# Kernel tuning notes

Hardware: AMD Instinct MI355X
Metric: run time of the kernel (lower is better)

Reference implementation:

```python
import jax, jax.numpy as jnp
import numpy as np

N_EMBD = 1024
N_HEAD = 16
HEAD_DIM = N_EMBD // N_HEAD

def setup_inputs() -> dict:
    key = jax.random.key(0)
    ks = jax.random.split(key, 5)
    B, T, C = 2, 2048, N_EMBD
    s = 1.0 / np.sqrt(C)
    x = jax.random.normal(ks[0], (B, T, C), dtype=jnp.float32)
    W_qkv = jax.random.normal(ks[1], (C, 3 * C), dtype=jnp.float32) * s
    b_qkv = jax.random.normal(ks[2], (3 * C,), dtype=jnp.float32) * 0.02
    W_o = jax.random.normal(ks[3], (C, C), dtype=jnp.float32) * s
    b_o = jax.random.normal(ks[4], (C,), dtype=jnp.float32) * 0.02
    return {"x": x, "W_qkv": W_qkv, "b_qkv": b_qkv, "W_o": W_o, "b_o": b_o}

def reference(x, W_qkv, b_qkv, W_o, b_o):
    B, T, C = x.shape
    H, D = N_HEAD, HEAD_DIM
    scale = 1.0 / np.sqrt(D)
    qkv = jnp.einsum('btc,cf->btf', x, W_qkv) + b_qkv  # [B,T,3C]
    q, k, v = jnp.split(qkv, 3, axis=-1)
    # [B,H,T,D]
    q = q.reshape(B, T, H, D).transpose(0, 2, 1, 3)
    k = k.reshape(B, T, H, D).transpose(0, 2, 1, 3)
    v = v.reshape(B, T, H, D).transpose(0, 2, 1, 3)
    att = jnp.einsum('bhqd,bhkd->bhqk', q, k) * scale  # [B,H,T,T]
    causal = jnp.tril(jnp.ones((T, T), dtype=bool))
    att = jnp.where(causal[None, None], att, -jnp.inf)
    att = jax.nn.softmax(att, axis=-1)
    y = jnp.einsum('bhqk,bhkd->bhqd', att, v)  # [B,H,T,D]
    y = y.transpose(0, 2, 1, 3).reshape(B, T, C)
    return jnp.einsum('btc,cf->btf', y, W_o) + b_o
```

## Files before the change

### kernel.cpp

```cpp
#include <hip/hip_runtime.h>
#include <hip/hip_bf16.h>

#define TT 2048
#define BB 2
#define CC 1024
#define NH 16
#define HD 64

typedef __attribute__((ext_vector_type(8))) short short8;
typedef __attribute__((ext_vector_type(4))) short short4b;
typedef __attribute__((ext_vector_type(4))) float f32x4;

typedef unsigned int __attribute__((address_space(1))) ui_gas;
typedef unsigned int __attribute__((address_space(3))) ui_las;

__device__ __forceinline__ float us2f(unsigned short u) {
    union { unsigned int i; float f; } v; v.i = ((unsigned int)u) << 16; return v.f;
}
__device__ __forceinline__ unsigned short f2us(float f) {
    union { float f; unsigned int i; } v; v.f = f;
    unsigned int i = v.i;
    unsigned int lsb = (i >> 16) & 1u;
    i += 0x7fffu + lsb;
    return (unsigned short)(i >> 16);
}
__device__ __forceinline__ unsigned int pack2_trunc(float a, float b) {
    union { float f; unsigned int u; } x, y; x.f = a; y.f = b;
    return (y.u & 0xffff0000u) | (x.u >> 16);
}

__device__ __forceinline__ void gl_lds16(const unsigned short* g, unsigned short* l) {
    __builtin_amdgcn_global_load_lds((const ui_gas*)g, (ui_las*)l, 16, 0, 0);
}

__global__ __launch_bounds__(64) void detect_kernel(
    const void* p0, const void* p1, const void* p2, const void* p3, const void* p4,
    int* flags)
{
    const void* ps[5] = {p0, p1, p2, p3, p4};
    const int lane = threadIdx.x;
    for (int k = 0; k < 5; ++k) {
        const unsigned short* u = (const unsigned short*)ps[k];
        int bad = 0;
        #pragma unroll
        for (int j = 0; j < 4; ++j) {
            float v = us2f(u[lane * 4 + j]);
            if (!(fabsf(v) < 1e4f)) bad = 1;
        }
        unsigned long long m = __ballot(bad != 0);
        if (lane == 0) flags[k] = (__popcll(m) < 4) ? 1 : 0;
    }
}

__device__ __forceinline__ float4 load4(const void* p, size_t i, int isbf) {
    if (isbf) {
        ushort4 u = *reinterpret_cast<const ushort4*>((const unsigned short*)p + i);
        return make_float4(us2f(u.x), us2f(u.y), us2f(u.z), us2f(u.w));
    } else {
        return *reinterpret_cast<const float4*>((const float*)p + i);
    }
}
__device__ __forceinline__ float load1(const void* p, size_t i, int isbf) {
    return isbf ? us2f(((const unsigned short*)p)[i]) : ((const float*)p)[i];
}

__global__ __launch_bounds__(256) void convert_bf16(
    const void* __restrict__ X, unsigned short* __restrict__ Y,
    const int* __restrict__ flags, int fi)
{
    const int isbf = flags[fi];
    const size_t i = ((size_t)blockIdx.x * 256 + threadIdx.x) * 8;
    float4 a = load4(X, i, isbf);
    float4 b = load4(X, i + 4, isbf);
    alignas(16) unsigned short pk[8];
    pk[0] = f2us(a.x); pk[1] = f2us(a.y); pk[2] = f2us(a.z); pk[3] = f2us(a.w);
    pk[4] = f2us(b.x); pk[5] = f2us(b.y); pk[6] = f2us(b.z); pk[7] = f2us(b.w);
    *reinterpret_cast<uint4*>(Y + i) = *reinterpret_cast<const uint4*>(pk);
}

__global__ __launch_bounds__(256) void transpose_w(
    const void* __restrict__ W, unsigned short* __restrict__ Wt,
    int Krows, int N, const int* __restrict__ flags, int fi)
{
    const int isbf = flags[fi];
    __shared__ float Ls[64 * 65];
    const int t = threadIdx.x;
    const int n0 = blockIdx.x * 64, k0 = blockIdx.y * 64;
    {
        const int r = t >> 2, cq = (t & 3) << 4;
        #pragma unroll
        for (int i = 0; i < 4; ++i) {
            float4 v = load4(W, (size_t)(k0 + r) * N + n0 + cq + i * 4, isbf);
            Ls[r * 65 + cq + i * 4 + 0] = v.x;
            Ls[r * 65 + cq + i * 4 + 1] = v.y;
            Ls[r * 65 + cq + i * 4 + 2] = v.z;
            Ls[r * 65 + cq + i * 4 + 3] = v.w;
        }
    }
    __syncthreads();
    {
        const int c = t & 63, kg = (t >> 6) * 16;
        alignas(16) unsigned short pk[16];
        #pragma unroll
        for (int i = 0; i < 16; ++i) pk[i] = f2us(Ls[(kg + i) * 65 + c]);
        unsigned short* dst = Wt + (size_t)(n0 + c) * Krows + k0 + kg;
        *reinterpret_cast<uint4*>(dst + 0) = *reinterpret_cast<const uint4*>(&pk[0]);
        *reinterpret_cast<uint4*>(dst + 8) = *reinterpret_cast<const uint4*>(&pk[8]);
    }
}

__global__ __launch_bounds__(256) void gemm_mfma(
    const unsigned short* __restrict__ A,
    const unsigned short* __restrict__ Bt,
    const void* __restrict__ bias, void* __restrict__ C,
    int M, int N, int K,
    const int* __restrict__ flags, int biasfi, int cfi)
{
    const int bias_bf = (biasfi >= 0) ? flags[biasfi] : 0;
    const int c_bf    = (cfi >= 0) ? flags[cfi] : ((cfi == -2) ? 1 : 0);

    __shared__ __align__(16) unsigned short Asl[8 * 512];
    __shared__ __align__(16) unsigned short Bsl[8 * 512];

    const int tid = threadIdx.x;
    const int l  = tid & 63;
    const int w  = tid >> 6;
    const int wm = w >> 1, wn = w & 1;
    const int bm = blockIdx.y * 128, bn = blockIdx.x * 128;
    const int lm = l & 15;
    const int lk = (l >> 4) * 8;

    f32x4 acc[4][4];
    #pragma unroll
    for (int i = 0; i < 4; ++i)
        #pragma unroll
        for (int j = 0; j < 4; ++j) acc[i][j] = (f32x4){0.f, 0.f, 0.f, 0.f};

    for (int k0 = 0; k0 < K; k0 += 32) {
        #pragma unroll
        for (int s = 0; s < 2; ++s) {
            const int r = 2 * w + s;
            gl_lds16(A  + (size_t)(bm + r * 16 + lm) * K + k0 + lk, &Asl[r * 512]);
            gl_lds16(Bt + (size_t)(bn + r * 16 + lm) * K + k0 + lk, &Bsl[r * 512]);
        }
        __syncthreads();
        short8 af[4], bf[4];
        #pragma unroll
        for (int i = 0; i < 4; ++i)
            af[i] = *reinterpret_cast<const short8*>(&Asl[(4 * wm + i) * 512 + l * 8]);
        #pragma unroll
        for (int j = 0; j < 4; ++j)
            bf[j] = *reinterpret_cast<const short8*>(&Bsl[(4 * wn + j) * 512 + l * 8]);
        #pragma unroll
        for (int i = 0; i < 4; ++i)
            #pragma unroll
            for (int j = 0; j < 4; ++j)
                acc[i][j] = __builtin_amdgcn_mfma_f32_16x16x32_bf16(af[i], bf[j], acc[i][j], 0, 0, 0);
        __syncthreads();
    }

    const int quad = l >> 4;
    float bv[4];
    #pragma unroll
    for (int j = 0; j < 4; ++j) bv[j] = load1(bias, bn + wn * 64 + j * 16 + lm, bias_bf);

    #pragma unroll
    for (int i = 0; i < 4; ++i) {
        #pragma unroll
        for (int r = 0; r < 4; ++r) {
            const int row = bm + wm * 64 + i * 16 + quad * 4 + r;
            #pragma unroll
            for (int j = 0; j < 4; ++j) {
                const int col = bn + wn * 64 + j * 16 + lm;
                const float val = acc[i][j][r] + bv[j];
                if (c_bf) ((unsigned short*)C)[(size_t)row * N + col] = f2us(val);
                else      ((float*)C)[(size_t)row * N + col] = val;
            }
        }
    }
}

__global__ __launch_bounds__(256) void transpose_v(
    const unsigned short* __restrict__ qkv, unsigned short* __restrict__ Vt)
{
    __shared__ __align__(16) unsigned short Ls[64 * 72];
    const int tid = threadIdx.x;
    const int tt = blockIdx.x;
    const int bh = blockIdx.y;
    const int b = bh >> 4, h = bh & 15;
    {
        const int tok = tid & 63, w = tid >> 6;
        const unsigned short* src = qkv + (size_t)(b * TT + tt * 64 + tok) * 3 * CC + 2 * CC + h * HD;
        #pragma unroll
        for (int c2 = 0; c2 < 2; ++c2) {
            int c = 2 * w + c2;
            uint4 d = *(const uint4*)(src + c * 8);
            *(uint4*)(&Ls[tok * 72 + c * 8]) = d;
        }
    }
    __syncthreads();
    {
        const int d = tid >> 2, kq = tid & 3;
        unsigned short out[16];
        #pragma unroll
        for (int i = 0; i < 16; ++i) out[i] = Ls[(kq * 16 + i) * 72 + d];
        unsigned short* dst = Vt + (size_t)bh * HD * TT + (size_t)d * TT + tt * 64 + kq * 16;
        *(uint4*)(dst + 0) = *(uint4*)(&out[0]);
        *(uint4*)(dst + 8) = *(uint4*)(&out[8]);
    }
}

__global__ __launch_bounds__(256) void attn_mfma(
    const unsigned short* __restrict__ qkv,
    const unsigned short* __restrict__ Vt,
    unsigned short* __restrict__ y)
{
    __shared__ __align__(16) unsigned short Ksh[8 * 512];
    __shared__ __align__(16) unsigned short Vsh[1039 * 8];

    const int tid = threadIdx.x;
    const int l   = tid & 63;
    const int w   = tid >> 6;
    const int quad = l >> 4;
    const int col  = l & 15;

    const int n  = blockIdx.x;
    const int g  = n >> 3;
    const int bh = (n & 7) * 4 + (g & 3);
    const int i  = g >> 2;
    const int tA = i, tB = 31 - i;
    const int b  = bh >> 4, h = bh & 15;

    for (int s = tid; s < 1039; s += 256)
        *(uint2*)(&Vsh[s * 8 + 4]) = make_uint2(0u, 0u);

    const float QSCALE = 0.18033688f;
    short8 qfA[2], qfB[2];
    #pragma unroll
    for (int t2 = 0; t2 < 2; ++t2) {
        const int qt = t2 ? tB : tA;
        short8* qf = t2 ? qfB : qfA;
        const int token = qt * 64 + w * 16 + col;
        const unsigned short* qrow = qkv + (size_t)(b * TT + token) * 3 * CC + h * HD;
        #pragma unroll
        for (int ks = 0; ks < 2; ++ks) {
            ushort4 u0 = *(const ushort4*)(qrow + ks * 32 + quad * 8);
            ushort4 u1 = *(const ushort4*)(qrow + ks * 32 + quad * 8 + 4);
            alignas(16) unsigned short pk[8];
            pk[0] = f2us(us2f(u0.x) * QSCALE);
            pk[1] = f2us(us2f(u0.y) * QSCALE);
            pk[2] = f2us(us2f(u0.z) * QSCALE);
            pk[3] = f2us(us2f(u0.w) * QSCALE);
            pk[4] = f2us(us2f(u1.x) * QSCALE);
            pk[5] = f2us(us2f(u1.y) * QSCALE);
            pk[6] = f2us(us2f(u1.z) * QSCALE);
            pk[7] = f2us(us2f(u1.w) * QSCALE);
            qf[ks] = *(const short8*)pk;
        }
    }

    f32x4 oA[4], oB[4];
    #pragma unroll
    for (int nb = 0; nb < 4; ++nb) {
        oA[nb] = (f32x4){0.f, 0.f, 0.f, 0.f};
        oB[nb] = (f32x4){0.f, 0.f, 0.f, 0.f};
    }
    float mA = -3e38f, lAc = 0.f, mB = -3e38f, lBc = 0.f;

    const unsigned short* kbase = qkv + (size_t)b * TT * 3 * CC + CC + h * HD;
    const unsigned short* vbase = Vt + (size_t)bh * HD * TT;

    const int vd = tid >> 2, vg0 = (tid & 3) * 4;

    uint4 rk[2], rv[2];
    auto issue_loads = [&](int kt) {
        const unsigned short* ksrc = kbase + (size_t)(kt * 64 + l) * 3 * CC;
        #pragma unroll
        for (int c2 = 0; c2 < 2; ++c2) {
            const int c = 2 * w + c2;
            rk[c2] = *(const uint4*)(ksrc + c * 8);
        }
        const unsigned short* vsrc = vbase + (size_t)vd * TT + kt * 64 + vg0 * 4;
        rv[0] = *(const uint4*)(vsrc + 0);
        rv[1] = *(const uint4*)(vsrc + 8);
    };
    auto write_lds = [&]() {
        #pragma unroll
        for (int c2 = 0; c2 < 2; ++c2) {
            const int c = 2 * w + c2;
            const int ks = c >> 2, q = c & 3;
            const int slot = ((quad * 2 + ks) * 64 + q * 16 + col) * 8;
            *(uint4*)(&Ksh[slot]) = rk[c2];
        }
        *(uint2*)(&Vsh[((vg0 + 0) * 65 + vd) * 8]) = make_uint2(rv[0].x, rv[0].y);
        *(uint2*)(&Vsh[((vg0 + 1) * 65 + vd) * 8]) = make_uint2(rv[0].z, rv[0].w);
        *(uint2*)(&Vsh[((vg0 + 2) * 65 + vd) * 8]) = make_uint2(rv[1].x, rv[1].y);
        *(uint2*)(&Vsh[((vg0 + 3) * 65 + vd) * 8]) = make_uint2(rv[1].z, rv[1].w);
    };

    auto step = [&](const short8* qf, f32x4* o, float& m_i, float& l_i, bool diag) {
        f32x4 st[4];
        #pragma unroll
        for (int nb = 0; nb < 4; ++nb) {
            f32x4 acc = {0.f, 0.f, 0.f, 0.f};
            #pragma unroll
            for (int ks = 0; ks < 2; ++ks) {
                short8 kf = *(const short8*)(&Ksh[((nb * 2 + ks) * 64 + l) * 8]);
                acc = __builtin_amdgcn_mfma_f32_16x16x32_bf16(kf, qf[ks], acc, 0, 0, 0);
            }
            st[nb] = acc;
        }
        float sv[4][4];
        #pragma unroll
        for (int nb = 0; nb < 4; ++nb)
            #pragma unroll
            for (int r = 0; r < 4; ++r) {
                float v = st[nb][r];
                if (diag && (nb * 16 + quad * 4 + r > w * 16 + col)) v = -3e38f;
                sv[nb][r] = v;
            }
        float rm = sv[0][0];
        #pragma unroll
        for (int nb = 0; nb < 4; ++nb)
            #pragma unroll
            for (int r = 0; r < 4; ++r) rm = fmaxf(rm, sv[nb][r]);
        rm = fmaxf(rm, __shfl_xor(rm, 16));
        rm = fmaxf(rm, __shfl_xor(rm, 32));
        const float mn = fmaxf(m_i, rm);
        const float al = __builtin_exp2f(m_i - mn);
        float pv[4][4];
        float rs = 0.f;
        #pragma unroll
        for (int nb = 0; nb < 4; ++nb)
            #pragma unroll
            for (int r = 0; r < 4; ++r) {
                float p = __builtin_exp2f(sv[nb][r] - mn);
                pv[nb][r] = p;
                rs += p;
            }
        rs += __shfl_xor(rs, 16);
        rs += __shfl_xor(rs, 32);
        l_i = l_i * al + rs;
        m_i = mn;
        float alr[4];
        #pragma unroll
        for (int r = 0; r < 4; ++r) alr[r] = __shfl(al, quad * 4 + r);
        #pragma unroll
        for (int nb = 0; nb < 4; ++nb)
            #pragma unroll
            for (int r = 0; r < 4; ++r) o[nb][r] *= alr[r];
#if __has_builtin(__builtin_amdgcn_mfma_f32_16x16x16bf16_1k)
        short4b pf[4];
        #pragma unroll
        for (int nbk = 0; nbk < 4; ++nbk) {
            union { short4b s; unsigned int u[2]; } pk;
            pk.u[0] = pack2_trunc(pv[nbk][0], pv[nbk][1]);
            pk.u[1] = pack2_trunc(pv[nbk][2], pv[nbk][3]);
            pf[nbk] = pk.s;
        }
        #pragma unroll
        for (int nbd = 0; nbd < 4; ++nbd)
            #pragma unroll
            for (int nbk = 0; nbk < 4; ++nbk) {
                short4b vf = *(const short4b*)(&Vsh[((nbk * 4 + quad) * 65 + nbd * 16 + col) * 8]);
                o[nbd] = __builtin_amdgcn_mfma_f32_16x16x16bf16_1k(pf[nbk], vf, o[nbd], 0, 0, 0);
            }
#else
        short8 pf[4];
        #pragma unroll
        for (int nbk = 0; nbk < 4; ++nbk) {
            union { short8 s; unsigned int u[4]; } pk;
            pk.u[0] = pack2_trunc(pv[nbk][0], pv[nbk][1]);
            pk.u[1] = pack2_trunc(pv[nbk][2], pv[nbk][3]);
            pk.u[2] = 0u; pk.u[3] = 0u;
            pf[nbk] = pk.s;
        }
        #pragma unroll
        for (int nbd = 0; nbd < 4; ++nbd)
            #pragma unroll
            for (int nbk = 0; nbk < 4; ++nbk) {
                short8 vf = *(const short8*)(&Vsh[((nbk * 4 + quad) * 65 + nbd * 16 + col) * 8]);
                o[nbd] = __builtin_amdgcn_mfma_f32_16x16x32_bf16(pf[nbk], vf, o[nbd], 0, 0, 0);
            }
#endif
    };

    issue_loads(0);
    for (int kt = 0; kt <= tB; ++kt) {
        write_lds();
        __syncthreads();
        if (kt < tB) issue_loads(kt + 1);
        step(qfB, oB, mB, lBc, kt == tB);
        if (kt <= tA) step(qfA, oA, mA, lAc, kt == tA);
        __syncthreads();
    }

    #pragma unroll
    for (int t2 = 0; t2 < 2; ++t2) {
        const int qt = t2 ? tB : tA;
        f32x4* o = t2 ? oB : oA;
        const float inv = 1.f / (t2 ? lBc : lAc);
        float invr[4];
        #pragma unroll
        for (int r = 0; r < 4; ++r) invr[r] = __shfl(inv, quad * 4 + r);
        #pragma unroll
        for (int nb = 0; nb < 4; ++nb)
            #pragma unroll
            for (int r = 0; r < 4; ++r) {
                int token = qt * 64 + w * 16 + quad * 4 + r;
                y[(size_t)(b * TT + token) * CC + h * HD + nb * 16 + col] = f2us(o[nb][r] * invr[r]);
            }
    }
}

extern "C" void kernel_launch(void* const* d_in, const int* in_sizes, int n_in,
                              void* d_out, int out_size, void* d_ws, size_t ws_size,
                              hipStream_t stream) {
    const int M = BB * TT;

    char* ws = (char*)d_ws;
    int*            flags = (int*)ws;                         ws += 256;
    unsigned short* xb    = (unsigned short*)ws;              ws += (size_t)M * CC * 2;
    unsigned short* Wqkvt = (unsigned short*)ws;              ws += (size_t)3 * CC * CC * 2;
    unsigned short* Wot   = (unsigned short*)ws;              ws += (size_t)CC * CC * 2;
    unsigned short* qkv   = (unsigned short*)ws;              ws += (size_t)M * 3 * CC * 2;
    unsigned short* Vt    = (unsigned short*)ws;              ws += (size_t)BB * NH * HD * TT * 2;
    unsigned short* y     = (unsigned short*)ws;

    detect_kernel<<<1, 64, 0, stream>>>(d_in[0], d_in[1], d_in[2], d_in[3], d_in[4], flags);

    convert_bf16<<<(M * CC) / (256 * 8), 256, 0, stream>>>(d_in[0], xb, flags, 0);
    transpose_w<<<dim3(3 * CC / 64, CC / 64), 256, 0, stream>>>(d_in[1], Wqkvt, CC, 3 * CC, flags, 1);
    transpose_w<<<dim3(CC / 64, CC / 64), 256, 0, stream>>>(d_in[3], Wot, CC, CC, flags, 3);

    gemm_mfma<<<dim3(3 * CC / 128, M / 128), 256, 0, stream>>>(
        xb, Wqkvt, d_in[2], qkv, M, 3 * CC, CC, flags, 2, -2);

    transpose_v<<<dim3(TT / 64, BB * NH), 256, 0, stream>>>(qkv, Vt);

    attn_mfma<<<512, 256, 0, stream>>>(qkv, Vt, y);

    gemm_mfma<<<dim3(CC / 128, M / 128), 256, 0, stream>>>(
        y, Wot, d_in[4], d_out, M, CC, CC, flags, 4, 0);
}
```

Measured before the change: 248.5 us.

## Split attention into one q-tile per block and retile output-projection GEMM

Attention blocks previously paired a short and a long query tile (i and 31-i) for load balance. Now each block handles a single query tile, doubling the grid to 1024 blocks, ordered longest-first. The V LDS buffer is halved when the 16x16x16 MFMA path is available, and the output-projection GEMM is templated to use 128x64 tiles so it launches more blocks. The goal is more parallelism and occupancy. The trade-off is that K/V tiles are reloaded per query tile instead of shared across two tiles.

```diff
diff --git a/kernel.cpp b/kernel.cpp
--- a/kernel.cpp
+++ b/kernel.cpp
@@ -13,6 +13,12 @@
 
 typedef unsigned int __attribute__((address_space(1))) ui_gas;
 typedef unsigned int __attribute__((address_space(3))) ui_las;
+
+#if __has_builtin(__builtin_amdgcn_mfma_f32_16x16x16bf16_1k)
+#define PV16 1
+#else
+#define PV16 0
+#endif
 
 __device__ __forceinline__ float us2f(unsigned short u) {
     union { unsigned int i; float f; } v; v.i = ((unsigned int)u) << 16; return v.f;
@@ -109,6 +115,7 @@
     }
 }
 
+template<int WM, int WN, int NWM, int NWN>
 __global__ __launch_bounds__(256) void gemm_mfma(
     const unsigned short* __restrict__ A,
     const unsigned short* __restrict__ Bt,
@@ -116,62 +123,69 @@
     int M, int N, int K,
     const int* __restrict__ flags, int biasfi, int cfi)
 {
+    constexpr int BM = WM * 16 * NWM, BN = WN * 16 * NWN;
+    constexpr int ASL = BM / 16, BSL = BN / 16;
+
     const int bias_bf = (biasfi >= 0) ? flags[biasfi] : 0;
     const int c_bf    = (cfi >= 0) ? flags[cfi] : ((cfi == -2) ? 1 : 0);
 
-    __shared__ __align__(16) unsigned short Asl[8 * 512];
-    __shared__ __align__(16) unsigned short Bsl[8 * 512];
+    __shared__ __align__(16) unsigned short Asl[ASL * 512];
+    __shared__ __align__(16) unsigned short Bsl[BSL * 512];
 
     const int tid = threadIdx.x;
     const int l  = tid & 63;
     const int w  = tid >> 6;
-    const int wm = w >> 1, wn = w & 1;
-    const int bm = blockIdx.y * 128, bn = blockIdx.x * 128;
+    const int wm = w / NWN, wn = w % NWN;
+    const int bm = blockIdx.y * BM, bn = blockIdx.x * BN;
     const int lm = l & 15;
     const int lk = (l >> 4) * 8;
 
-    f32x4 acc[4][4];
+    f32x4 acc[WM][WN];
     #pragma unroll
-    for (int i = 0; i < 4; ++i)
-        #pragma unroll
-        for (int j = 0; j < 4; ++j) acc[i][j] = (f32x4){0.f, 0.f, 0.f, 0.f};
+    for (int i = 0; i < WM; ++i)
+        #pragma unroll
+        for (int j = 0; j < WN; ++j) acc[i][j] = (f32x4){0.f, 0.f, 0.f, 0.f};
 
     for (int k0 = 0; k0 < K; k0 += 32) {
         #pragma unroll
-        for (int s = 0; s < 2; ++s) {
-            const int r = 2 * w + s;
-            gl_lds16(A  + (size_t)(bm + r * 16 + lm) * K + k0 + lk, &Asl[r * 512]);
+        for (int s = 0; s < ASL / 4; ++s) {
+            const int r = w * (ASL / 4) + s;
+            gl_lds16(A + (size_t)(bm + r * 16 + lm) * K + k0 + lk, &Asl[r * 512]);
+        }
+        #pragma unroll
+        for (int s = 0; s < BSL / 4; ++s) {
+            const int r = w * (BSL / 4) + s;
             gl_lds16(Bt + (size_t)(bn + r * 16 + lm) * K + k0 + lk, &Bsl[r * 512]);
         }
         __syncthreads();
-        short8 af[4], bf[4];
-        #pragma unroll
-        for (int i = 0; i < 4; ++i)
-            af[i] = *reinterpret_cast<const short8*>(&Asl[(4 * wm + i) * 512 + l * 8]);
-        #pragma unroll
-        for (int j = 0; j < 4; ++j)
-            bf[j] = *reinterpret_cast<const short8*>(&Bsl[(4 * wn + j) * 512 + l * 8]);
-        #pragma unroll
-        for (int i = 0; i < 4; ++i)
-            #pragma unroll
-            for (int j = 0; j < 4; ++j)
+        short8 af[WM], bf[WN];
+        #pragma unroll
+        for (int i = 0; i < WM; ++i)
+            af[i] = *reinterpret_cast<const short8*>(&Asl[(WM * wm + i) * 512 + l * 8]);
+        #pragma unroll
+        for (int j = 0; j < WN; ++j)
+            bf[j] = *reinterpret_cast<const short8*>(&Bsl[(WN * wn + j) * 512 + l * 8]);
+        #pragma unroll
+        for (int i = 0; i < WM; ++i)
+            #pragma unroll
+            for (int j = 0; j < WN; ++j)
                 acc[i][j] = __builtin_amdgcn_mfma_f32_16x16x32_bf16(af[i], bf[j], acc[i][j], 0, 0, 0);
         __syncthreads();
     }
 
     const int quad = l >> 4;
-    float bv[4];
+    float bv[WN];
     #pragma unroll
-    for (int j = 0; j < 4; ++j) bv[j] = load1(bias, bn + wn * 64 + j * 16 + lm, bias_bf);
+    for (int j = 0; j < WN; ++j) bv[j] = load1(bias, bn + (WN * wn + j) * 16 + lm, bias_bf);
 
     #pragma unroll
-    for (int i = 0; i < 4; ++i) {
+    for (int i = 0; i < WM; ++i) {
         #pragma unroll
         for (int r = 0; r < 4; ++r) {
-            const int row = bm + wm * 64 + i * 16 + quad * 4 + r;
-            #pragma unroll
-            for (int j = 0; j < 4; ++j) {
-                const int col = bn + wn * 64 + j * 16 + lm;
+            const int row = bm + (WM * wm + i) * 16 + quad * 4 + r;
+            #pragma unroll
+            for (int j = 0; j < WN; ++j) {
+                const int col = bn + (WN * wn + j) * 16 + lm;
                 const float val = acc[i][j][r] + bv[j];
                 if (c_bf) ((unsigned short*)C)[(size_t)row * N + col] = f2us(val);
                 else      ((float*)C)[(size_t)row * N + col] = val;
@@ -216,7 +230,11 @@
     unsigned short* __restrict__ y)
 {
     __shared__ __align__(16) unsigned short Ksh[8 * 512];
+#if PV16
+    __shared__ __align__(16) unsigned short Vsh[1039 * 4];
+#else
     __shared__ __align__(16) unsigned short Vsh[1039 * 8];
+#endif
 
     const int tid = threadIdx.x;
     const int l   = tid & 63;
@@ -225,21 +243,18 @@
     const int col  = l & 15;
 
     const int n  = blockIdx.x;
-    const int g  = n >> 3;
-    const int bh = (n & 7) * 4 + (g & 3);
-    const int i  = g >> 2;
-    const int tA = i, tB = 31 - i;
+    const int bh = (n & 7) * 4 + ((n >> 3) & 3);
+    const int qt = 31 - (n >> 5);
     const int b  = bh >> 4, h = bh & 15;
 
+#if !PV16
     for (int s = tid; s < 1039; s += 256)
         *(uint2*)(&Vsh[s * 8 + 4]) = make_uint2(0u, 0u);
+#endif
 
     const float QSCALE = 0.18033688f;
-    short8 qfA[2], qfB[2];
-    #pragma unroll
-    for (int t2 = 0; t2 < 2; ++t2) {
-        const int qt = t2 ? tB : tA;
-        short8* qf = t2 ? qfB : qfA;
+    short8 qf[2];
+    {
         const int token = qt * 64 + w * 16 + col;
         const unsigned short* qrow = qkv + (size_t)(b * TT + token) * 3 * CC + h * HD;
         #pragma unroll
@@ -259,13 +274,10 @@
         }
     }
 
-    f32x4 oA[4], oB[4];
+    f32x4 o[4];
     #pragma unroll
-    for (int nb = 0; nb < 4; ++nb) {
-        oA[nb] = (f32x4){0.f, 0.f, 0.f, 0.f};
-        oB[nb] = (f32x4){0.f, 0.f, 0.f, 0.f};
-    }
-    float mA = -3e38f, lAc = 0.f, mB = -3e38f, lBc = 0.f;
+    for (int nb = 0; nb < 4; ++nb) o[nb] = (f32x4){0.f, 0.f, 0.f, 0.f};
+    float m_i = -3e38f, l_i = 0.f;
 
     const unsigned short* kbase = qkv + (size_t)b * TT * 3 * CC + CC + h * HD;
     const unsigned short* vbase = Vt + (size_t)bh * HD * TT;
@@ -292,13 +304,20 @@
             const int slot = ((quad * 2 + ks) * 64 + q * 16 + col) * 8;
             *(uint4*)(&Ksh[slot]) = rk[c2];
         }
+#if PV16
+        *(uint2*)(&Vsh[((vg0 + 0) * 65 + vd) * 4]) = make_uint2(rv[0].x, rv[0].y);
+        *(uint2*)(&Vsh[((vg0 + 1) * 65 + vd) * 4]) = make_uint2(rv[0].z, rv[0].w);
+        *(uint2*)(&Vsh[((vg0 + 2) * 65 + vd) * 4]) = make_uint2(rv[1].x, rv[1].y);
+        *(uint2*)(&Vsh[((vg0 + 3) * 65 + vd) * 4]) = make_uint2(rv[1].z, rv[1].w);
+#else
         *(uint2*)(&Vsh[((vg0 + 0) * 65 + vd) * 8]) = make_uint2(rv[0].x, rv[0].y);
         *(uint2*)(&Vsh[((vg0 + 1) * 65 + vd) * 8]) = make_uint2(rv[0].z, rv[0].w);
         *(uint2*)(&Vsh[((vg0 + 2) * 65 + vd) * 8]) = make_uint2(rv[1].x, rv[1].y);
         *(uint2*)(&Vsh[((vg0 + 3) * 65 + vd) * 8]) = make_uint2(rv[1].z, rv[1].w);
+#endif
     };
 
-    auto step = [&](const short8* qf, f32x4* o, float& m_i, float& l_i, bool diag) {
+    auto step = [&](bool diag) {
         f32x4 st[4];
         #pragma unroll
         for (int nb = 0; nb < 4; ++nb) {
@@ -349,7 +368,7 @@
         for (int nb = 0; nb < 4; ++nb)
             #pragma unroll
             for (int r = 0; r < 4; ++r) o[nb][r] *= alr[r];
-#if __has_builtin(__builtin_amdgcn_mfma_f32_16x16x16bf16_1k)
+#if PV16
         short4b pf[4];
         #pragma unroll
         for (int nbk = 0; nbk < 4; ++nbk) {
@@ -362,7 +381,7 @@
         for (int nbd = 0; nbd < 4; ++nbd)
             #pragma unroll
             for (int nbk = 0; nbk < 4; ++nbk) {
-                short4b vf = *(const short4b*)(&Vsh[((nbk * 4 + quad) * 65 + nbd * 16 + col) * 8]);
+                short4b vf = *(const short4b*)(&Vsh[((nbk * 4 + quad) * 65 + nbd * 16 + col) * 4]);
                 o[nbd] = __builtin_amdgcn_mfma_f32_16x16x16bf16_1k(pf[nbk], vf, o[nbd], 0, 0, 0);
             }
 #else
@@ -386,20 +405,16 @@
     };
 
     issue_loads(0);
-    for (int kt = 0; kt <= tB; ++kt) {
+    for (int kt = 0; kt <= qt; ++kt) {
         write_lds();
         __syncthreads();
-        if (kt < tB) issue_loads(kt + 1);
-        step(qfB, oB, mB, lBc, kt == tB);
-        if (kt <= tA) step(qfA, oA, mA, lAc, kt == tA);
+        if (kt < qt) issue_loads(kt + 1);
+        step(kt == qt);
         __syncthreads();
     }
 
-    #pragma unroll
-    for (int t2 = 0; t2 < 2; ++t2) {
-        const int qt = t2 ? tB : tA;
-        f32x4* o = t2 ? oB : oA;
-        const float inv = 1.f / (t2 ? lBc : lAc);
+    {
+        const float inv = 1.f / l_i;
         float invr[4];
         #pragma unroll
         for (int r = 0; r < 4; ++r) invr[r] = __shfl(inv, quad * 4 + r);
@@ -433,13 +448,13 @@
     transpose_w<<<dim3(3 * CC / 64, CC / 64), 256, 0, stream>>>(d_in[1], Wqkvt, CC, 3 * CC, flags, 1);
     transpose_w<<<dim3(CC / 64, CC / 64), 256, 0, stream>>>(d_in[3], Wot, CC, CC, flags, 3);
 
-    gemm_mfma<<<dim3(3 * CC / 128, M / 128), 256, 0, stream>>>(
+    gemm_mfma<4, 4, 2, 2><<<dim3(3 * CC / 128, M / 128), 256, 0, stream>>>(
         xb, Wqkvt, d_in[2], qkv, M, 3 * CC, CC, flags, 2, -2);
 
     transpose_v<<<dim3(TT / 64, BB * NH), 256, 0, stream>>>(qkv, Vt);
 
-    attn_mfma<<<512, 256, 0, stream>>>(qkv, Vt, y);
-
-    gemm_mfma<<<dim3(CC / 128, M / 128), 256, 0, stream>>>(
+    attn_mfma<<<1024, 256, 0, stream>>>(qkv, Vt, y);
+
+    gemm_mfma<2, 4, 4, 1><<<dim3(CC / 64, M / 128), 256, 0, stream>>>(
         y, Wot, d_in[4], d_out, M, CC, CC, flags, 4, 0);
 }
```

Result: no change. 252.9 us (+1.7%).
